# Kernel tuning notes

Hardware: AMD Instinct MI355X
Metric: run time of the kernel (lower is better)

## Reference

```python
import jax, jax.numpy as jnp
import numpy as np

C1, C2, C3 = 64, 256, 256
HEADS, WS = 8, 7
HD = C3 // HEADS
PAD = WS // 2
SCALE = HD ** -0.5
EPS = 1e-5


def _layernorm(x, gamma, beta):
    mu = jnp.mean(x, axis=-1, keepdims=True)
    var = jnp.var(x, axis=-1, keepdims=True)
    return (x - mu) * jax.lax.rsqrt(var + EPS) * gamma + beta


def setup_inputs() -> dict:
    key = jax.random.key(0)
    ks = jax.random.split(key, 12)
    B, H, W = 2, 200, 200
    s = 0.02
    return {
        "F_lidar": jax.random.normal(ks[0], (B, C1, H, W), jnp.float32),
        "F_cam": jax.random.normal(ks[1], (B, C2, H, W), jnp.float32),
        "Wq": jax.random.normal(ks[2], (C3, C1), jnp.float32) * s,
        "Wk": jax.random.normal(ks[3], (C3, C2), jnp.float32) * s,
        "Wv": jax.random.normal(ks[4], (C3, C2), jnp.float32) * s,
        "Wo": jax.random.normal(ks[5], (C3, C3), jnp.float32) * s,
        "Wr": jax.random.normal(ks[6], (C3, C1), jnp.float32) * s,
        "g1": jnp.ones((C3,), jnp.float32),
        "b1": jnp.zeros((C3,), jnp.float32),
        "g2": jnp.ones((C3,), jnp.float32),
        "b2": jnp.zeros((C3,), jnp.float32),
        "W1": jax.random.normal(ks[7], (C3, 4 * C3), jnp.float32) * s,
        "bf1": jnp.zeros((4 * C3,), jnp.float32),
        "W2": jax.random.normal(ks[8], (4 * C3, C3), jnp.float32) * s,
        "bf2": jnp.zeros((C3,), jnp.float32),
    }


def reference(F_lidar, F_cam, Wq, Wk, Wv, Wo, Wr, g1, b1, g2, b2, W1, bf1, W2, bf2):
    B, _, H, W = F_lidar.shape
    # 1x1 conv projections (no bias)
    Q = jnp.einsum('oc,bchw->bohw', Wq, F_lidar)
    K = jnp.einsum('oc,bchw->bohw', Wk, F_cam)
    V = jnp.einsum('oc,bchw->bohw', Wv, F_cam)
    # replicate padding (torch 'replicate' == jnp 'edge')
    Kp = jnp.pad(K, ((0, 0), (0, 0), (PAD, PAD), (PAD, PAD)), mode='edge')
    Vp = jnp.pad(V, ((0, 0), (0, 0), (PAD, PAD), (PAD, PAD)), mode='edge')
    Qm = Q.reshape(B, HEADS, HD, H, W)
    # local-window attention logits without materializing the unfolded (C*49) tensor:
    # loop over the 49 fixed window offsets, accumulating per-offset dot products.
    logits = []
    for i in range(WS):
        for j in range(WS):
            Km = Kp[:, :, i:i + H, j:j + W].reshape(B, HEADS, HD, H, W)
            logits.append(jnp.einsum('bndhw,bndhw->bnhw', Qm, Km))
    logits = jnp.stack(logits, axis=-1) * SCALE          # (B, heads, H, W, 49)
    attn = jax.nn.softmax(logits, axis=-1)
    out = jnp.zeros_like(Qm)
    k = 0
    for i in range(WS):
        for j in range(WS):
            Vm = Vp[:, :, i:i + H, j:j + W].reshape(B, HEADS, HD, H, W)
            out = out + attn[..., k][:, :, None] * Vm
            k += 1
    out = out.reshape(B, C3, H, W)
    out = jnp.einsum('oc,bchw->bohw', Wo, out)
    residual = jnp.einsum('oc,bchw->bohw', Wr, F_lidar)
    x = (residual + out).transpose(0, 2, 3, 1)           # (B, H, W, C3)
    x = _layernorm(x, g1, b1)
    # FFN (dropout is identity in eval)
    y = jax.nn.relu(jnp.dot(x, W1) + bf1)
    y = jnp.dot(y, W2) + bf2
    x = _layernorm(x + y, g2, b2)
    return x.transpose(0, 3, 1, 2)
```

## Files before the change

kernel.cpp:

```cpp
#include <hip/hip_runtime.h>
#include <stdint.h>

#define HH 200
#define WW 200
#define HWSZ 40000
#define NPX 80000

typedef __attribute__((ext_vector_type(8))) short bf16x8;
typedef __attribute__((ext_vector_type(4))) float f32x4;

__device__ __forceinline__ float bf2f(unsigned short u) {
    union { uint32_t i; float f; } c; c.i = ((uint32_t)u) << 16; return c.f;
}
__device__ __forceinline__ unsigned short f2bf(float f) {
    union { float f; uint32_t i; } c; c.f = f;
    uint32_t r = c.i + 0x7FFF + ((c.i >> 16) & 1);
    return (unsigned short)(r >> 16);
}
__device__ __forceinline__ unsigned int cvtpk_bf16(float lo, float hi) {
    unsigned int r;
    asm("v_cvt_pk_bf16_f32 %0, %1, %2" : "=v"(r) : "v"(lo), "v"(hi));
    return r;
}
__device__ __forceinline__ void gload16(const void* g, void* l) {
    __builtin_amdgcn_global_load_lds(
        (const __attribute__((address_space(1))) unsigned int*)g,
        (__attribute__((address_space(3))) unsigned int*)l, 16, 0, 0);
}

__global__ __launch_bounds__(256) void cvt_weights(
    const float* __restrict__ Wq, const float* __restrict__ Wk,
    const float* __restrict__ Wv, const float* __restrict__ Wo,
    const float* __restrict__ Wr, const float* __restrict__ W1,
    const float* __restrict__ W2,
    unsigned short* Wq_b, unsigned short* Wk_b, unsigned short* Wv_b,
    unsigned short* Wcat, unsigned short* W1t, unsigned short* W2t)
{
    const int seg = blockIdx.y;
    const int idx = blockIdx.x * 256 + threadIdx.x;
    if (seg == 0)      { if (idx < 16384) Wq_b[idx] = f2bf(Wq[idx]); }
    else if (seg == 1) { if (idx < 65536) Wk_b[idx] = f2bf(Wk[idx]); }
    else if (seg == 2) { if (idx < 65536) Wv_b[idx] = f2bf(Wv[idx]); }
    else if (seg == 3) {
        if (idx < 81920) {
            int r = idx / 320, k = idx - r * 320;
            Wcat[idx] = f2bf(k < 256 ? Wo[r * 256 + k] : Wr[r * 64 + (k - 256)]);
        }
    } else if (seg == 4) {
        if (idx < 262144) { int o = idx >> 8, i = idx & 255; W1t[idx] = f2bf(W1[i * 1024 + o]); }
    } else {
        if (idx < 262144) { int o = idx >> 10, i = idx & 1023; W2t[idx] = f2bf(W2[i * 256 + o]); }
    }
}

__global__ __launch_bounds__(256) void to_nhwc(
    const float* __restrict__ src, unsigned short* __restrict__ dst, int C)
{
    __shared__ unsigned short T[64][72];
    const int b = blockIdx.z, c0 = blockIdx.y * 64, px0 = blockIdx.x * 64;
    const int t = threadIdx.x;
    const int pxl = t & 63, cl0 = t >> 6;
    const float* sp = src + ((size_t)(b * C + c0 + cl0)) * HWSZ + px0 + pxl;
    #pragma unroll
    for (int i = 0; i < 16; ++i)
        T[pxl][cl0 + i * 4] = f2bf(sp[(size_t)i * 4 * HWSZ]);
    __syncthreads();
    #pragma unroll
    for (int r = 0; r < 2; ++r) {
        int idx = t + r * 256;
        int p = idx >> 3, cof = (idx & 7) * 8;
        uint4 v = *(const uint4*)&T[p][cof];
        *(uint4*)(dst + ((size_t)(b * HWSZ + px0 + p)) * C + c0 + cof) = v;
    }
}

__global__ __launch_bounds__(256) void gemm_bf16(
    const unsigned short* __restrict__ In, int inStride,
    const unsigned short* __restrict__ In2, int in2Stride, int K1,
    const unsigned short* __restrict__ Wb, int wStride, int Ktot,
    unsigned short* __restrict__ OutB, float* __restrict__ OutF,
    const float* __restrict__ bias, int flags, int outStride)
{
    __shared__ bf16x8 AB[2][1024];
    const int t = threadIdx.x;
    int bx = blockIdx.x, by = blockIdx.y;
    if (flags & 4) {
        const int nxy = gridDim.x * gridDim.y;
        const int flat = blockIdx.x + gridDim.x * blockIdx.y;
        const int qq = nxy >> 3, rr = nxy & 7;
        const int xcd = flat & 7, idx = flat >> 3;
        const int w2 = (xcd < rr ? xcd * (qq + 1)
                                 : rr * (qq + 1) + (xcd - rr) * qq) + idx;
        by = w2 % gridDim.y;
        bx = w2 / gridDim.y;
    }
    const int px0 = bx * 128;
    const int n0 = by * 128;
    const int lane = t & 63, w = t >> 6;
    const int mh = w & 1, nh = w >> 1;

    f32x4 acc[4][4] = {};

    auto STAGE = [&](int buf, int k0s) {
        #pragma unroll
        for (int r = 0; r < 2; ++r) {
            const int c = t + r * 256;
            const int l = c & 63;
            const int ko = k0s + ((l >> 4) << 3);
            const int mt = c >> 6;
            {
                const int px = px0 + mt * 16 + (l & 15);
                const unsigned short* sp = (ko < K1)
                    ? (In  + (size_t)px * inStride  + ko)
                    : (In2 + (size_t)px * in2Stride + (ko - K1));
                gload16(sp, &AB[buf][c]);
            }
            {
                const int cc = n0 + mt * 16 + (l & 15);
                gload16(Wb + (size_t)cc * wStride + ko, &AB[buf][512 + c]);
            }
        }
    };

    STAGE(0, 0);
    __syncthreads();
    int cur = 0;

    for (int k0 = 0; k0 < Ktot; k0 += 32) {
        if (k0 + 32 < Ktot) STAGE(cur ^ 1, k0 + 32);
        bf16x8 av[4], bv[4];
        #pragma unroll
        for (int i = 0; i < 4; ++i) av[i] = AB[cur][(mh * 4 + i) * 64 + lane];
        #pragma unroll
        for (int j = 0; j < 4; ++j) bv[j] = AB[cur][512 + (nh * 4 + j) * 64 + lane];
        #pragma unroll
        for (int i = 0; i < 4; ++i)
            #pragma unroll
            for (int j = 0; j < 4; ++j)
                acc[i][j] = __builtin_amdgcn_mfma_f32_16x16x32_bf16(
                    av[i], bv[j], acc[i][j], 0, 0, 0);
        __syncthreads();
        cur ^= 1;
    }

    const int q = lane >> 4, ln = lane & 15;
    const bool relu = (flags & 1) != 0, accum = (flags & 2) != 0;
    #pragma unroll
    for (int i = 0; i < 4; ++i) {
        #pragma unroll
        for (int j = 0; j < 4; ++j) {
            const int coutv = n0 + nh * 64 + j * 16 + ln;
            const float bval = bias ? bias[coutv] : 0.0f;
            #pragma unroll
            for (int r = 0; r < 4; ++r) {
                const int px = px0 + mh * 64 + i * 16 + q * 4 + r;
                float v = acc[i][j][r] + bval;
                if (relu) v = fmaxf(v, 0.0f);
                if (OutB) {
                    OutB[(size_t)px * outStride + coutv] = f2bf(v);
                } else {
                    float* op = OutF + (size_t)px * 256 + coutv;
                    if (accum) v += *op;
                    *op = v;
                }
            }
        }
    }
}

__global__ __launch_bounds__(512) void ffn2_ln2(
    const unsigned short* __restrict__ Y1,
    const unsigned short* __restrict__ XLb,
    const unsigned short* __restrict__ W2t,
    const float* __restrict__ bf2v,
    const float* __restrict__ g2, const float* __restrict__ b2,
    float* __restrict__ Out)
{
    __shared__ union {
        bf16x8 AB[2][1536];
        float  T[256 * 33];
    } sm;
    __shared__ float part_s[4][128], part_q[4][128];

    const int t = threadIdx.x;
    const int px0 = blockIdx.x * 128;
    const int lane = t & 63, w = t >> 6;
    const int mh = w & 1, nh = w >> 1;
    const int q = lane >> 4, ln = lane & 15;

    f32x4 acc[4][4] = {};

    auto STAGE = [&](int buf, int k0s) {
        #pragma unroll
        for (int r = 0; r < 3; ++r) {
            const int c = t + r * 512;
            const int l = c & 63;
            const int ko = k0s + ((l >> 4) << 3);
            if (c < 512) {
                const int mt = c >> 6;
                const int px = px0 + mt * 16 + (l & 15);
                gload16(Y1 + (size_t)px * 1024 + ko, &sm.AB[buf][c]);
            } else {
                const int c2 = c - 512;
                const int nt = c2 >> 6;
                const int cc = nt * 16 + (l & 15);
                gload16(W2t + (size_t)cc * 1024 + ko, &sm.AB[buf][c]);
            }
        }
    };

    STAGE(0, 0);
    __syncthreads();
    int cur = 0;

    for (int k0 = 0; k0 < 1024; k0 += 32) {
        if (k0 + 32 < 1024) STAGE(cur ^ 1, k0 + 32);
        bf16x8 av[4], bv[4];
        #pragma unroll
        for (int i = 0; i < 4; ++i) av[i] = sm.AB[cur][(mh * 4 + i) * 64 + lane];
        #pragma unroll
        for (int j = 0; j < 4; ++j) bv[j] = sm.AB[cur][512 + (nh * 4 + j) * 64 + lane];
        #pragma unroll
        for (int i = 0; i < 4; ++i)
            #pragma unroll
            for (int j = 0; j < 4; ++j)
                acc[i][j] = __builtin_amdgcn_mfma_f32_16x16x32_bf16(
                    av[i], bv[j], acc[i][j], 0, 0, 0);
        __syncthreads();
        cur ^= 1;
    }

    float biasv[4], gv[4], bvv[4];
    #pragma unroll
    for (int j = 0; j < 4; ++j) {
        const int col = nh * 64 + j * 16 + ln;
        biasv[j] = bf2v[col];
        gv[j] = g2[col];
        bvv[j] = b2[col];
    }

    #pragma unroll
    for (int i = 0; i < 4; ++i) {
        #pragma unroll
        for (int r = 0; r < 4; ++r) {
            const int pl = mh * 64 + i * 16 + q * 4 + r;
            const size_t px = (size_t)px0 + pl;
            float s = 0.0f, ssq = 0.0f;
            #pragma unroll
            for (int j = 0; j < 4; ++j) {
                const int col = nh * 64 + j * 16 + ln;
                float v = acc[i][j][r] + biasv[j] + bf2f(XLb[px * 256 + col]);
                acc[i][j][r] = v;
                s += v; ssq += v * v;
            }
            #pragma unroll
            for (int o = 1; o <= 8; o <<= 1) {
                s += __shfl_xor(s, o); ssq += __shfl_xor(ssq, o);
            }
            if (ln == 0) { part_s[nh][pl] = s; part_q[nh][pl] = ssq; }
        }
    }
    __syncthreads();

    float muv[4][4], rsv[4][4];
    #pragma unroll
    for (int i = 0; i < 4; ++i) {
        #pragma unroll
        for (int r = 0; r < 4; ++r) {
            const int pl = mh * 64 + i * 16 + q * 4 + r;
            const float s  = part_s[0][pl] + part_s[1][pl] + part_s[2][pl] + part_s[3][pl];
            const float sq = part_q[0][pl] + part_q[1][pl] + part_q[2][pl] + part_q[3][pl];
            const float mu = s * (1.0f / 256.0f);
            muv[i][r] = mu;
            rsv[i][r] = rsqrtf(sq * (1.0f / 256.0f) - mu * mu + 1e-5f);
        }
    }
    __syncthreads();

    #pragma unroll
    for (int ck = 0; ck < 4; ++ck) {
        if (mh == (ck >> 1)) {
            const int ib = (ck & 1) * 2;
            #pragma unroll
            for (int ii = 0; ii < 2; ++ii) {
                const int i = ib + ii;
                #pragma unroll
                for (int j = 0; j < 4; ++j) {
                    const int col = nh * 64 + j * 16 + ln;
                    #pragma unroll
                    for (int r = 0; r < 4; ++r) {
                        sm.T[col * 33 + ii * 16 + q * 4 + r] =
                            (acc[i][j][r] - muv[i][r]) * rsv[i][r] * gv[j] + bvv[j];
                    }
                }
            }
        }
        __syncthreads();
        const int pxc = px0 + ck * 32;
        const int bb = pxc / HWSZ;
        const int hw0 = pxc - bb * HWSZ;
        #pragma unroll
        for (int p = 0; p < 16; ++p) {
            const int idx = t + p * 512;
            const int c = idx >> 5, pxl = idx & 31;
            Out[((size_t)(bb * 256 + c)) * HWSZ + hw0 + pxl] = sm.T[c * 33 + pxl];
        }
        __syncthreads();
    }
}

__global__ __launch_bounds__(256) void attn_bf16(
    const unsigned short* Q, const unsigned short* __restrict__ K,
    const unsigned short* __restrict__ V, unsigned short* A)
{
    __shared__ __align__(16) unsigned short vt[32 * 536];
    const int flat = blockIdx.x + 169 * (blockIdx.y + 8 * blockIdx.z);
    const int wsz = (flat & 7) * 338 + (flat >> 3);
    const int tile = wsz >> 4, rem = wsz & 15;
    const int head = rem >> 1, b = rem & 1;
    const int tiy = tile / 13, tix = tile - tiy * 13;
    const int h0 = tiy * 16, w0 = tix * 16;
    const int t = threadIdx.x;
    const int lane = t & 63, wv = t >> 6;
    const int g = lane >> 4, n = lane & 15;
    const int co = head * 32;
    const size_t pxb = (size_t)b * HWSZ;

    for (int idx = t; idx < 832; idx += 256) {
        if (idx < 704) {
            int ch = idx / 22, r = idx - ch * 22;
            *(unsigned int*)&vt[ch * 536 + r * 24 + 22] = 0u;
        } else {
            int k2 = idx - 704;
            int ch = k2 >> 2, e = k2 & 3;
            *(unsigned int*)&vt[ch * 536 + 528 + e * 2] = 0u;
        }
    }
    for (int idx = t; idx < 484 * 4; idx += 256) {
        int pos = idx >> 2, chunk = idx & 3;
        int r = pos / 22, c = pos - r * 22;
        int gh = min(max(h0 + r - 3, 0), HH - 1);
        int gw = min(max(w0 + c - 3, 0), WW - 1);
        bf16x8 v8 = *(const bf16x8*)(V + (pxb + gh * WW + gw) * 256 + co + chunk * 8);
        unsigned short* dp = &vt[(chunk * 8) * 536 + r * 24 + c];
        #pragma unroll
        for (int e = 0; e < 8; ++e) dp[e * 536] = (unsigned short)v8[e];
    }
    __syncthreads();

    const f32x4 z4 = {0.f, 0.f, 0.f, 0.f};
    const int qw  = min(w0 + n, WW - 1);
    const int kc0 = min(max(w0 - 3 + n, 0), WW - 1);
    const int kc1 = min(w0 + 13 + n, WW - 1);
    const bool hi2 = (g >> 1) != 0;
    const int src0 = ((g & 1) * 2) * 16 + n;
    const int src1 = src0 + 16;

    for (int hh = 0; hh < 4; ++hh) {
        const int hl = wv * 4 + hh;
        const int h = h0 + hl;
        const int hc = min(h, HH - 1);

        const bf16x8 qf = *(const bf16x8*)(Q + (pxb + hc * WW + qw) * 256 + co + g * 8);

        f32x4 s0[7], s1[7];
        #pragma unroll
        for (int i = 0; i < 7; ++i) {
            const int gh = min(max(h - 3 + i, 0), HH - 1);
            const unsigned short* kr = K + (pxb + gh * WW) * 256 + co + g * 8;
            bf16x8 a0 = *(const bf16x8*)(kr + (size_t)kc0 * 256);
            bf16x8 a1 = *(const bf16x8*)(kr + (size_t)kc1 * 256);
            s0[i] = __builtin_amdgcn_mfma_f32_16x16x32_bf16(a0, qf, z4, 0, 0, 0);
            s1[i] = __builtin_amdgcn_mfma_f32_16x16x32_bf16(a1, qf, z4, 0, 0, 0);
        }

        float mx = -3.0e38f;
        #pragma unroll
        for (int r = 0; r < 4; ++r) {
            float m0 = s0[0][r], m1 = s1[0][r];
            #pragma unroll
            for (int i = 1; i < 7; ++i) {
                m0 = fmaxf(m0, s0[i][r]);
                m1 = fmaxf(m1, s1[i][r]);
            }
            const int k0 = 4 * g + r, k1 = k0 + 16;
            mx = fmaxf(mx, ((unsigned)(k0 - n) <= 6u) ? m0 : -3.0e38f);
            mx = fmaxf(mx, ((unsigned)(k1 - n) <= 6u) ? m1 : -3.0e38f);
        }
        mx = fmaxf(mx, __shfl_xor(mx, 16));
        mx = fmaxf(mx, __shfl_xor(mx, 32));

        float sum = 0.0f;
        #pragma unroll
        for (int r = 0; r < 4; ++r) {
            const int k0 = 4 * g + r, k1 = k0 + 16;
            const bool in0 = (unsigned)(k0 - n) <= 6u;
            const bool in1 = (unsigned)(k1 - n) <= 6u;
            #pragma unroll
            for (int i = 0; i < 7; ++i) {
                float e0 = in0 ? __expf((s0[i][r] - mx) * 0.17677669529663687f) : 0.0f;
                float e1 = in1 ? __expf((s1[i][r] - mx) * 0.17677669529663687f) : 0.0f;
                s0[i][r] = e0; s1[i][r] = e1;
                sum += e0 + e1;
            }
        }
        sum += __shfl_xor(sum, 16);
        sum += __shfl_xor(sum, 32);
        const float inv = __builtin_amdgcn_rcpf(sum);

        unsigned int pa[7], pb[7], pc[7], pd[7];
        #pragma unroll
        for (int i = 0; i < 7; ++i) {
            pa[i] = cvtpk_bf16(s0[i][0] * inv, s0[i][1] * inv);
            pb[i] = cvtpk_bf16(s0[i][2] * inv, s0[i][3] * inv);
            pc[i] = cvtpk_bf16(s1[i][0] * inv, s1[i][1] * inv);
            pd[i] = cvtpk_bf16(s1[i][2] * inv, s1[i][3] * inv);
        }

        f32x4 acc0 = z4, acc1 = z4;
        #pragma unroll
        for (int i = 0; i < 7; ++i) {
            const int a0s = __shfl((int)pa[i], src0);
            const int c0s = __shfl((int)pc[i], src0);
            const int b0s = __shfl((int)pb[i], src0);
            const int d0s = __shfl((int)pd[i], src0);
            const int a1s = __shfl((int)pa[i], src1);
            const int c1s = __shfl((int)pc[i], src1);
            const int b1s = __shfl((int)pb[i], src1);
            const int d1s = __shfl((int)pd[i], src1);
            union { unsigned int u[4]; bf16x8 v; } pu;
            pu.u[0] = (unsigned int)(hi2 ? c0s : a0s);
            pu.u[1] = (unsigned int)(hi2 ? d0s : b0s);
            pu.u[2] = (unsigned int)(hi2 ? c1s : a1s);
            pu.u[3] = (unsigned int)(hi2 ? d1s : b1s);
            const unsigned short* vr = &vt[(hl + i) * 24 + g * 8];
            bf16x8 vf0 = *(const bf16x8*)(vr + n * 536);
            bf16x8 vf1 = *(const bf16x8*)(vr + (n + 16) * 536);
            acc0 = __builtin_amdgcn_mfma_f32_16x16x32_bf16(pu.v, vf0, acc0, 0, 0, 0);
            acc1 = __builtin_amdgcn_mfma_f32_16x16x32_bf16(pu.v, vf1, acc1, 0, 0, 0);
        }

        if (h < HH) {
            unsigned short* ap = A + (pxb + h * WW) * 256 + co + n;
            const int wp = w0 + g * 4;
            #pragma unroll
            for (int r = 0; r < 4; ++r) {
                if (wp + r < WW) {
                    ap[(size_t)(wp + r) * 256]      = f2bf(acc0[r]);
                    ap[(size_t)(wp + r) * 256 + 16] = f2bf(acc1[r]);
                }
            }
        }
    }
}

__global__ __launch_bounds__(256) void ln1_k(
    const float* __restrict__ X, const float* __restrict__ g,
    const float* __restrict__ bt, unsigned short* __restrict__ XLb)
{
    const int wv = threadIdx.x >> 6, lane = threadIdx.x & 63;
    const size_t px = (size_t)blockIdx.x * 4 + wv;
    const float4 v = *(const float4*)(X + px * 256 + lane * 4);
    float s = v.x + v.y + v.z + v.w;
    float ss = v.x * v.x + v.y * v.y + v.z * v.z + v.w * v.w;
    #pragma unroll
    for (int o = 32; o; o >>= 1) { s += __shfl_xor(s, o); ss += __shfl_xor(ss, o); }
    const float mu = s * (1.0f / 256.0f);
    const float var = ss * (1.0f / 256.0f) - mu * mu;
    const float rs = rsqrtf(var + 1e-5f);
    const float4 gv = *(const float4*)(g + lane * 4);
    const float4 bv = *(const float4*)(bt + lane * 4);
    ushort4 o4;
    o4.x = f2bf((v.x - mu) * rs * gv.x + bv.x);
    o4.y = f2bf((v.y - mu) * rs * gv.y + bv.y);
    o4.z = f2bf((v.z - mu) * rs * gv.z + bv.z);
    o4.w = f2bf((v.w - mu) * rs * gv.w + bv.w);
    *(ushort4*)(XLb + px * 256 + lane * 4) = o4;
}

extern "C" void kernel_launch(void* const* d_in, const int* in_sizes, int n_in,
                              void* d_out, int out_size, void* d_ws, size_t ws_size,
                              hipStream_t stream)
{
    const float* F_lidar = (const float*)d_in[0];
    const float* F_cam   = (const float*)d_in[1];
    const float* Wq  = (const float*)d_in[2];
    const float* Wk  = (const float*)d_in[3];
    const float* Wv  = (const float*)d_in[4];
    const float* Wo  = (const float*)d_in[5];
    const float* Wr  = (const float*)d_in[6];
    const float* g1  = (const float*)d_in[7];
    const float* b1  = (const float*)d_in[8];
    const float* g2  = (const float*)d_in[9];
    const float* b2  = (const float*)d_in[10];
    const float* W1  = (const float*)d_in[11];
    const float* bf1 = (const float*)d_in[12];
    const float* W2  = (const float*)d_in[13];
    const float* bf2 = (const float*)d_in[14];

    char* wsb = (char*)d_ws;
    unsigned short* Fl  = (unsigned short*)(wsb);
    unsigned short* Fc  = (unsigned short*)(wsb + 10240000);
    unsigned short* Qb  = (unsigned short*)(wsb + 51200000);
    unsigned short* Kb  = (unsigned short*)(wsb + 92160000);
    unsigned short* Vb  = (unsigned short*)(wsb + 133120000);
    unsigned short* Y1b = Fc;
    unsigned short* XLb = (unsigned short*)(wsb + 174080000);
    unsigned short* Wq_b = (unsigned short*)(wsb + 215040000);
    unsigned short* Wk_b = Wq_b + 16384;
    unsigned short* Wv_b = Wk_b + 65536;
    unsigned short* Wcat = Wv_b + 65536;
    unsigned short* W1t  = Wcat + 81920;
    unsigned short* W2t  = W1t + 262144;
    float* XW  = (float*)d_out;
    float* out = (float*)d_out;

    const dim3 blk(256);

    cvt_weights<<<dim3(1024, 6), blk, 0, stream>>>(Wq, Wk, Wv, Wo, Wr, W1, W2,
        Wq_b, Wk_b, Wv_b, Wcat, W1t, W2t);
    to_nhwc<<<dim3(625, 1, 2), blk, 0, stream>>>(F_lidar, Fl, 64);
    to_nhwc<<<dim3(625, 4, 2), blk, 0, stream>>>(F_cam, Fc, 256);

    gemm_bf16<<<dim3(625, 2), blk, 0, stream>>>(Fl, 64, Fl, 64, 64,
        Wq_b, 64, 64, Qb, nullptr, nullptr, 4, 256);
    gemm_bf16<<<dim3(625, 2), blk, 0, stream>>>(Fc, 256, Fc, 256, 256,
        Wk_b, 256, 256, Kb, nullptr, nullptr, 4, 256);
    gemm_bf16<<<dim3(625, 2), blk, 0, stream>>>(Fc, 256, Fc, 256, 256,
        Wv_b, 256, 256, Vb, nullptr, nullptr, 4, 256);

    attn_bf16<<<dim3(169, 8, 2), blk, 0, stream>>>(Qb, Kb, Vb, Qb);

    gemm_bf16<<<dim3(625, 2), blk, 0, stream>>>(Qb, 256, Fl, 64, 256,
        Wcat, 320, 320, nullptr, XW, nullptr, 4, 256);

    ln1_k<<<dim3(20000), blk, 0, stream>>>(XW, g1, b1, XLb);

    gemm_bf16<<<dim3(625, 8), blk, 0, stream>>>(XLb, 256, XLb, 256, 256,
        W1t, 256, 256, Y1b, nullptr, bf1, 5, 1024);

    ffn2_ln2<<<dim3(625), dim3(512), 0, stream>>>(Y1b, XLb, W2t, bf2, g2, b2, out);
}
```

Before: 693.5 us.

## Prefetch GEMM K-tiles two stages ahead with explicit vmcnt waits

Both MFMA GEMM kernels now issue the first two K-tiles up front, so two tiles are always in flight. Each iteration waits on vmcnt only for the older tile, reads its fragments into registers, then refills the freed buffer before running the MFMAs. This removes the full __syncthreads drain on every K step and lets global-to-LDS copies overlap compute more deeply. The FFN2 kernel also hoists its bias and LayerNorm parameter loads ahead of the main loop. The risk is that the hand-counted vmcnt values and barrier placement must stay in sync with the number of loads each stage issues.

```diff
diff --git a/kernel.cpp b/kernel.cpp
--- a/kernel.cpp
+++ b/kernel.cpp
@@ -8,6 +8,11 @@
 
 typedef __attribute__((ext_vector_type(8))) short bf16x8;
 typedef __attribute__((ext_vector_type(4))) float f32x4;
+
+#define VM_WAIT(N) asm volatile("s_waitcnt vmcnt(" #N ")" ::: "memory")
+#define LGKM_WAIT0 asm volatile("s_waitcnt lgkmcnt(0)" ::: "memory")
+#define BARRIER()  __builtin_amdgcn_s_barrier()
+#define SCHED_FENCE() __builtin_amdgcn_sched_barrier(0)
 
 __device__ __forceinline__ float bf2f(unsigned short u) {
     union { uint32_t i; float f; } c; c.i = ((uint32_t)u) << 16; return c.f;
@@ -122,25 +127,45 @@
         }
     };
 
+    const int nsteps = Ktot >> 5;
     STAGE(0, 0);
-    __syncthreads();
+    if (nsteps > 1) STAGE(1, 32);
     int cur = 0;
 
-    for (int k0 = 0; k0 < Ktot; k0 += 32) {
-        if (k0 + 32 < Ktot) STAGE(cur ^ 1, k0 + 32);
+    for (int s = 0; s < nsteps - 1; ++s) {
+        VM_WAIT(4);
+        BARRIER();
         bf16x8 av[4], bv[4];
         #pragma unroll
         for (int i = 0; i < 4; ++i) av[i] = AB[cur][(mh * 4 + i) * 64 + lane];
         #pragma unroll
         for (int j = 0; j < 4; ++j) bv[j] = AB[cur][512 + (nh * 4 + j) * 64 + lane];
+        LGKM_WAIT0;
+        BARRIER();
+        SCHED_FENCE();
+        if (s + 2 < nsteps) STAGE(cur, (s + 2) * 32);
         #pragma unroll
         for (int i = 0; i < 4; ++i)
             #pragma unroll
             for (int j = 0; j < 4; ++j)
                 acc[i][j] = __builtin_amdgcn_mfma_f32_16x16x32_bf16(
                     av[i], bv[j], acc[i][j], 0, 0, 0);
-        __syncthreads();
         cur ^= 1;
+    }
+    VM_WAIT(0);
+    BARRIER();
+    {
+        bf16x8 av[4], bv[4];
+        #pragma unroll
+        for (int i = 0; i < 4; ++i) av[i] = AB[cur][(mh * 4 + i) * 64 + lane];
+        #pragma unroll
+        for (int j = 0; j < 4; ++j) bv[j] = AB[cur][512 + (nh * 4 + j) * 64 + lane];
+        #pragma unroll
+        for (int i = 0; i < 4; ++i)
+            #pragma unroll
+            for (int j = 0; j < 4; ++j)
+                acc[i][j] = __builtin_amdgcn_mfma_f32_16x16x32_bf16(
+                    av[i], bv[j], acc[i][j], 0, 0, 0);
     }
 
     const int q = lane >> 4, ln = lane & 15;
@@ -187,6 +212,15 @@
     const int lane = t & 63, w = t >> 6;
     const int mh = w & 1, nh = w >> 1;
     const int q = lane >> 4, ln = lane & 15;
+
+    float biasv[4], gv[4], bvv[4];
+    #pragma unroll
+    for (int j = 0; j < 4; ++j) {
+        const int col = nh * 64 + j * 16 + ln;
+        biasv[j] = bf2v[col];
+        gv[j] = g2[col];
+        bvv[j] = b2[col];
+    }
 
     f32x4 acc[4][4] = {};
 
@@ -210,33 +244,43 @@
     };
 
     STAGE(0, 0);
-    __syncthreads();
+    STAGE(1, 32);
     int cur = 0;
 
-    for (int k0 = 0; k0 < 1024; k0 += 32) {
-        if (k0 + 32 < 1024) STAGE(cur ^ 1, k0 + 32);
+    for (int s = 0; s < 31; ++s) {
+        VM_WAIT(3);
+        BARRIER();
         bf16x8 av[4], bv[4];
         #pragma unroll
         for (int i = 0; i < 4; ++i) av[i] = sm.AB[cur][(mh * 4 + i) * 64 + lane];
         #pragma unroll
         for (int j = 0; j < 4; ++j) bv[j] = sm.AB[cur][512 + (nh * 4 + j) * 64 + lane];
+        LGKM_WAIT0;
+        BARRIER();
+        SCHED_FENCE();
+        if (s + 2 < 32) STAGE(cur, (s + 2) * 32);
         #pragma unroll
         for (int i = 0; i < 4; ++i)
             #pragma unroll
             for (int j = 0; j < 4; ++j)
                 acc[i][j] = __builtin_amdgcn_mfma_f32_16x16x32_bf16(
                     av[i], bv[j], acc[i][j], 0, 0, 0);
-        __syncthreads();
         cur ^= 1;
     }
-
-    float biasv[4], gv[4], bvv[4];
-    #pragma unroll
-    for (int j = 0; j < 4; ++j) {
-        const int col = nh * 64 + j * 16 + ln;
-        biasv[j] = bf2v[col];
-        gv[j] = g2[col];
-        bvv[j] = b2[col];
+    VM_WAIT(0);
+    BARRIER();
+    {
+        bf16x8 av[4], bv[4];
+        #pragma unroll
+        for (int i = 0; i < 4; ++i) av[i] = sm.AB[cur][(mh * 4 + i) * 64 + lane];
+        #pragma unroll
+        for (int j = 0; j < 4; ++j) bv[j] = sm.AB[cur][512 + (nh * 4 + j) * 64 + lane];
+        #pragma unroll
+        for (int i = 0; i < 4; ++i)
+            #pragma unroll
+            for (int j = 0; j < 4; ++j)
+                acc[i][j] = __builtin_amdgcn_mfma_f32_16x16x32_bf16(
+                    av[i], bv[j], acc[i][j], 0, 0, 0);
     }
 
     #pragma unroll
```

Result: no change. 682.5 us (-1.6%).
